# Optimization experiments

Hardware: AMD Instinct MI355X
Metric: run time of the kernel (lower is better)

The kernel has to match this reference:

```python
import jax, jax.numpy as jnp
import numpy as np

B, S, D_MODEL, NUM_HEADS, DFF = 4, 2048, 256, 8, 1024
DEPTH = D_MODEL // NUM_HEADS
EPS = 1e-6
LENGTH_SCALE = 1.0


def setup_inputs() -> dict:
    key = jax.random.key(0)
    ks = jax.random.split(key, 18)
    n = lambda k, shp, s=0.05: (jax.random.normal(k, shp, dtype=jnp.float32) * s)
    return {
        "x": jax.random.normal(ks[0], (B, S, D_MODEL), dtype=jnp.float32),
        "wq_w": n(ks[1], (D_MODEL, D_MODEL)), "wq_b": jnp.zeros((D_MODEL,), jnp.float32),
        "wk_w": n(ks[2], (D_MODEL, D_MODEL)), "wk_b": jnp.zeros((D_MODEL,), jnp.float32),
        "wv_w": n(ks[3], (D_MODEL, D_MODEL)), "wv_b": jnp.zeros((D_MODEL,), jnp.float32),
        "wo_w": n(ks[4], (D_MODEL, D_MODEL)), "wo_b": jnp.zeros((D_MODEL,), jnp.float32),
        "ffn1_w": n(ks[5], (D_MODEL, DFF)), "ffn1_b": jnp.zeros((DFF,), jnp.float32),
        "ffn2_w": n(ks[6], (DFF, D_MODEL)), "ffn2_b": jnp.zeros((D_MODEL,), jnp.float32),
        "ln1_g": jnp.ones((D_MODEL,), jnp.float32), "ln1_b": jnp.zeros((D_MODEL,), jnp.float32),
        "ln2_g": jnp.ones((D_MODEL,), jnp.float32), "ln2_b": jnp.zeros((D_MODEL,), jnp.float32),
    }


def _layernorm(x, g, b):
    mu = jnp.mean(x, axis=-1, keepdims=True)
    var = jnp.mean(jnp.square(x - mu), axis=-1, keepdims=True)
    return (x - mu) * jax.lax.rsqrt(var + EPS) * g + b


def _split_heads(t):
    # [B,S,D_MODEL] -> [B,H,S,depth]
    return t.reshape(B, S, NUM_HEADS, DEPTH).transpose(0, 2, 1, 3)


def _encoder_layer(x, wq_w, wq_b, wk_w, wk_b, wv_w, wv_b, wo_w, wo_b,
                   ffn1_w, ffn1_b, ffn2_w, ffn2_b, ln1_g, ln1_b, ln2_g, ln2_b):
    q = _split_heads(x @ wq_w + wq_b)
    k = _split_heads(x @ wk_w + wk_b)
    v = _split_heads(x @ wv_w + wv_b)
    # pairwise squared distances: ||q||^2 - 2 q.k + ||k||^2 -> [B,H,S,S]
    q2 = jnp.sum(q * q, axis=-1)  # [B,H,S]
    k2 = jnp.sum(k * k, axis=-1)  # [B,H,S]
    dists = q2[..., :, None] - 2.0 * jnp.einsum("bhqd,bhkd->bhqk", q, k) + k2[..., None, :]
    # exponentiated-quadratic kernel, then softmax over keys (mask=None)
    attn = jax.nn.softmax(jnp.exp(-0.5 * dists / (LENGTH_SCALE ** 2)), axis=-1)
    out = jnp.einsum("bhqk,bhkd->bhqd", attn, v)  # [B,H,S,depth]
    out = out.transpose(0, 2, 1, 3).reshape(B, S, D_MODEL)
    attn_out = out @ wo_w + wo_b
    # dropout is identity (training=False)
    out1 = _layernorm(x + attn_out, ln1_g, ln1_b)
    ffn = jax.nn.relu(out1 @ ffn1_w + ffn1_b) @ ffn2_w + ffn2_b
    return _layernorm(out1 + ffn, ln2_g, ln2_b)


def reference(x, wq_w, wq_b, wk_w, wk_b, wv_w, wv_b, wo_w, wo_b,
              ffn1_w, ffn1_b, ffn2_w, ffn2_b, ln1_g, ln1_b, ln2_g, ln2_b):
    return _encoder_layer(x, wq_w, wq_b, wk_w, wk_b, wv_w, wv_b, wo_w, wo_b,
                          ffn1_w, ffn1_b, ffn2_w, ffn2_b, ln1_g, ln1_b, ln2_g, ln2_b)
```

## Files before the change

kernel.cpp:

```cpp
#include <hip/hip_runtime.h>
#include <hip/hip_bf16.h>

#define SQL  2048
#define DM   256
#define LNEPS 1e-6f
#define LOG2E    (1.44269504f)

#define B_XB    (0ull)
#define B_QB    (4ull<<20)
#define B_KB    (8ull<<20)
#define B_VT    (12ull<<20)
#define B_CTX   (16ull<<20)
#define B_O1B   (20ull<<20)
#define B_O1F   (24ull<<20)
#define B_MID   (32ull<<20)
#define B_WQKVT (48ull<<20)
#define B_WOT   ((48ull<<20)+(512ull<<10))
#define B_W1T   (49ull<<20)
#define B_W2T   ((49ull<<20)+(512ull<<10))
#define B_BQKV  (50ull<<20)
#define B_HQ    ((50ull<<20)+(64ull<<10))
#define B_HK    ((50ull<<20)+(320ull<<10))
#define B_C2    (0ull)

typedef float  f32x16 __attribute__((ext_vector_type(16)));
typedef short  bf16x8 __attribute__((ext_vector_type(8)));
typedef int    i32x4  __attribute__((ext_vector_type(4)));
typedef int    i32x2  __attribute__((ext_vector_type(2)));

static __device__ __forceinline__ unsigned short bfu(float f){
    __hip_bfloat16 h = __float2bfloat16(f);
    return *reinterpret_cast<unsigned short*>(&h);
}
static __device__ __forceinline__ unsigned pk2(float a, float b){
    return (unsigned)bfu(a) | ((unsigned)bfu(b) << 16);
}
static __device__ __forceinline__ void glds16(const void* g, void* l){
    __builtin_amdgcn_global_load_lds((const __attribute__((address_space(1))) unsigned int*)g,
                                     (__attribute__((address_space(3))) unsigned int*)l, 16, 0, 0);
}

__global__ __launch_bounds__(256) void k_packall(
    const float* __restrict__ wq, const float* __restrict__ wk, const float* __restrict__ wv,
    const float* __restrict__ wo, const float* __restrict__ w1, const float* __restrict__ w2,
    const float* __restrict__ bq, const float* __restrict__ bk, const float* __restrict__ bv,
    const float* __restrict__ x,
    unsigned short* __restrict__ wqkvT, unsigned short* __restrict__ woT,
    unsigned short* __restrict__ w1T, unsigned short* __restrict__ w2T,
    float* __restrict__ bqkv, unsigned short* __restrict__ xb)
{
    __shared__ float tile[32][33];
    const int bid = blockIdx.x;
    const int t = threadIdx.x;
    if (bid < 768) {
        const float* W; unsigned short* Wt; int K, N, xk, yn;
        if (bid < 192) {
            int which = bid >> 6, local = bid & 63;
            W = (which == 0) ? wq : (which == 1 ? wk : wv);
            Wt = wqkvT + which * 65536; K = 256; N = 256;
            xk = local & 7; yn = local >> 3;
        } else if (bid < 256) {
            int local = bid - 192; W = wo; Wt = woT; K = 256; N = 256;
            xk = local & 7; yn = local >> 3;
        } else if (bid < 512) {
            int local = bid - 256; W = w1; Wt = w1T; K = 256; N = 1024;
            xk = local & 7; yn = local >> 3;
        } else {
            int local = bid - 512; W = w2; Wt = w2T; K = 1024; N = 256;
            xk = local & 31; yn = local >> 5;
        }
        const int tx = t & 31, ty = t >> 5;
        const int kb = xk * 32, nb = yn * 32;
#pragma unroll
        for (int i = 0; i < 32; i += 8) tile[ty + i][tx] = W[(size_t)(kb + ty + i) * N + nb + tx];
        __syncthreads();
#pragma unroll
        for (int i = 0; i < 32; i += 8) Wt[(size_t)(nb + ty + i) * K + kb + tx] = bfu(tile[tx][ty + i]);
    } else if (bid < 771) {
        int wb = bid - 768;
        const float* s = (wb == 0) ? bq : (wb == 1 ? bk : bv);
        bqkv[wb * 256 + t] = s[t];
    } else {
        const int i = (bid - 771) * 256 + t;
        float4 v = ((const float4*)x)[i];
        ushort4 o; o.x = bfu(v.x); o.y = bfu(v.y); o.z = bfu(v.z); o.w = bfu(v.w);
        ((ushort4*)xb)[i] = o;
    }
}

__global__ __launch_bounds__(256, 4) void k_qkv(
    const unsigned short* __restrict__ A, const unsigned short* __restrict__ Bt,
    const float* __restrict__ bias,
    unsigned short* __restrict__ qb, unsigned short* __restrict__ kb,
    char* __restrict__ vtg,
    unsigned int* __restrict__ hqp, unsigned int* __restrict__ hkp)
{
    __shared__ __align__(16) char As[8192];
    __shared__ __align__(16) char Bs[16384];
    const int t = threadIdx.x;
    const int lane = t & 63, w = t >> 6;
    const int lo = lane & 31, hi = lane >> 5;
    const int row0 = blockIdx.x * 64;
    const int col0 = blockIdx.y * 128;
    const int mr = (w & 1) * 32, nc = (w >> 1) * 64;
    f32x16 acc[2] = {};

    for (int kt = 0; kt < 4; ++kt) {
        const int k0 = kt * 64;
#pragma unroll
        for (int it = 0; it < 2; ++it) {
            const int idx = it * 256 + t;
            const int r = idx >> 3, g = idx & 7;
            glds16((const char*)(A + (size_t)(row0 + r) * 256 + k0) + ((g ^ (r & 7)) << 4),
                   As + it * 4096 + w * 1024 + lane * 16);
        }
#pragma unroll
        for (int it = 0; it < 4; ++it) {
            const int idx = it * 256 + t;
            const int r = idx >> 3, g = idx & 7;
            glds16((const char*)(Bt + (size_t)(col0 + r) * 256 + k0) + ((g ^ (r & 7)) << 4),
                   Bs + it * 4096 + w * 1024 + lane * 16);
        }
        __syncthreads();
        const int rA = mr + lo;
        const int rB = nc + lo;
#pragma unroll
        for (int s = 0; s < 4; ++s) {
            const int g = s * 2 + hi;
            bf16x8 fa  = *(const bf16x8*)(As + rA * 128 + ((g ^ (rA & 7)) << 4));
            bf16x8 fb0 = *(const bf16x8*)(Bs + rB * 128 + ((g ^ (rB & 7)) << 4));
            bf16x8 fb1 = *(const bf16x8*)(Bs + (rB + 32) * 128 + ((g ^ (rB & 7)) << 4));
            acc[0] = __builtin_amdgcn_mfma_f32_32x32x16_bf16(fa, fb0, acc[0], 0, 0, 0);
            acc[1] = __builtin_amdgcn_mfma_f32_32x32x16_bf16(fa, fb1, acc[1], 0, 0, 0);
        }
        __syncthreads();
    }
#pragma unroll
    for (int n = 0; n < 2; ++n) {
        const int c0 = col0 + nc + n * 32;
        const int which = c0 >> 8, h = (c0 >> 5) & 7;
        const float bv = bias[c0 + lo];
        if (which < 2) {
            unsigned short* dst = (which == 0) ? qb : kb;
            const float scl = (which == 0) ? LOG2E : 1.0f;
#pragma unroll
            for (int r = 0; r < 16; ++r) {
                const int gr = row0 + mr + (r & 3) + 8 * (r >> 2) + 4 * hi;
                const int b = gr >> 11, s = gr & 2047;
                const unsigned short u = bfu((acc[n][r] + bv) * scl);
                dst[(((size_t)(b * 8 + h)) * SQL + s) * 32 + lo] = u;
                const float vr = __builtin_bit_cast(float, ((unsigned)u) << 16);
                float sv = vr * vr;
                sv += __shfl_xor(sv, 1);  sv += __shfl_xor(sv, 2);
                sv += __shfl_xor(sv, 4);  sv += __shfl_xor(sv, 8);
                sv += __shfl_xor(sv, 16);
                if (lo == 0) {
                    const size_t gi = (size_t)(b * 8 + h) * SQL + s;
                    if (which == 0)
                        hqp[gi] = 0x3F80u | ((unsigned)bfu(-0.34657359f * sv + 0.52876637f) << 16);
                    else
                        hkp[gi] = (unsigned)bfu(-0.72134752f * sv) | 0x3F800000u;
                }
            }
        } else {
#pragma unroll
            for (int r = 0; r < 16; ++r) {
                const int gr = row0 + mr + (r & 3) + 8 * (r >> 2) + 4 * hi;
                const int b = gr >> 11, s = gr & 2047;
                const int o = s * 2;
                const int op = (o & ~0x78) | ((((o >> 3) & 15) ^ (lo & 15)) << 3);
                *(unsigned short*)(vtg + ((size_t)(b * 8 + h)) * 131072 + (size_t)lo * 4096 + op)
                    = bfu(acc[n][r] + bv);
            }
        }
    }
}

__global__ __launch_bounds__(512, 4) void k_attn(
    const unsigned short* __restrict__ qg, const unsigned short* __restrict__ kg,
    const char* __restrict__ vtg, const unsigned int* __restrict__ hqp,
    const unsigned int* __restrict__ hkp, unsigned short* __restrict__ ctxb)
{
    __shared__ __align__(16) char smem[34048];
    char* kls = smem;
    char* vtl = smem + 16384;
    float* hks  = (float*)(smem + 32768);
    float* invs = (float*)(smem + 33792);
    float* redacc = (float*)smem;
    float* redden = (float*)(smem + 24576);

    const int t = threadIdx.x;
    const int grp = t >> 7;
    const int tl  = t & 127;
    const int lane = t & 63;
    const int w   = (t >> 6) & 1;
    const int lo = lane & 31;
    const int hi = lane >> 5;

    const int bid = (blockIdx.x & 7) * 128 + (blockIdx.x >> 3);
    const int qc = bid & 31;
    const int bh = bid >> 5;

    const int qrow = qc * 64 + w * 32 + lo;
    const unsigned short* qp = qg + ((size_t)bh * SQL + qrow) * 32;
    const bf16x8 qf0 = *(const bf16x8*)(qp + hi * 8);
    const bf16x8 qf1 = *(const bf16x8*)(qp + 16 + hi * 8);
    i32x4 b3i = {};
    if (hi == 0) b3i[0] = (int)hqp[(size_t)bh * SQL + qrow];
    const bf16x8 b3 = __builtin_bit_cast(bf16x8, b3i);

    f32x16 acc = {};
    float den = 0.f;

    const unsigned short* kbg = kg + (size_t)bh * SQL * 32;
    const char* vtb = vtg + (size_t)bh * 131072;
    const unsigned int* hkb = hkp + (size_t)bh * SQL;
    char* kd = kls + grp * 4096;
    char* vd = vtl + grp * 4096;

    for (int kt = 0; kt < 8; ++kt) {
        const int key0 = grp * 512 + kt * 64;
        {
#pragma unroll
            for (int it = 0; it < 2; ++it) {
                const int idx = it * 128 + tl;
                const int r = idx >> 2, gl = idx & 3;
                glds16((const char*)(kbg + (size_t)(key0 + r) * 32) + ((gl ^ ((r >> 1) & 3)) << 4),
                       kd + idx * 16);
                const int vrw = idx >> 3, vch = idx & 7;
                glds16(vtb + (size_t)vrw * 4096 + key0 * 2 + vch * 16, vd + idx * 16);
            }
            if (tl < 64) hks[grp * 64 + tl] = __builtin_bit_cast(float, hkb[key0 + tl]);
        }
        __syncthreads();

#pragma unroll
        for (int h2 = 0; h2 < 2; ++h2) {
            const int kb32 = h2 * 32;
            const int kA = kb32 + lo;
            const char* krow = kd + kA * 64;
            const int ksw = (kA >> 1) & 3;
            bf16x8 kf0 = *(const bf16x8*)(krow + (((0 + hi) ^ ksw) << 4));
            bf16x8 kf1 = *(const bf16x8*)(krow + (((2 + hi) ^ ksw) << 4));
            i32x4 a3i = {};
            if (hi == 0) a3i[0] = __builtin_bit_cast(int, hks[grp * 64 + kA]);
            f32x16 sc = {};
            __builtin_amdgcn_s_setprio(1);
            sc = __builtin_amdgcn_mfma_f32_32x32x16_bf16(kf0, qf0, sc, 0, 0, 0);
            sc = __builtin_amdgcn_mfma_f32_32x32x16_bf16(kf1, qf1, sc, 0, 0, 0);
            sc = __builtin_amdgcn_mfma_f32_32x32x16_bf16(
                     __builtin_bit_cast(bf16x8, a3i), b3, sc, 0, 0, 0);
            __builtin_amdgcn_s_setprio(0);
            float wv[16];
#pragma unroll
            for (int r = 0; r < 16; ++r) {
                float e1 = __builtin_amdgcn_exp2f(sc[r]);
                float ww = __builtin_amdgcn_exp2f(e1);
                den += ww;
                wv[r] = ww;
            }
            i32x4 p0; p0[0]=pk2(wv[0],wv[1]);   p0[1]=pk2(wv[2],wv[3]);
                      p0[2]=pk2(wv[4],wv[5]);   p0[3]=pk2(wv[6],wv[7]);
            i32x4 p1; p1[0]=pk2(wv[8],wv[9]);   p1[1]=pk2(wv[10],wv[11]);
                      p1[2]=pk2(wv[12],wv[13]); p1[3]=pk2(wv[14],wv[15]);
            const char* vrow = vd + lo * 128;
            const int vxor = (lo & 15) << 3;
            const int o0 = (kb32 + 4 * hi) * 2;
            const int o1 = (kb32 + 16 + 4 * hi) * 2;
            i32x2 a0 = *(const i32x2*)(vrow + (o0 ^ vxor));
            i32x2 a1 = *(const i32x2*)(vrow + ((o0 + 16) ^ vxor));
            i32x2 b0 = *(const i32x2*)(vrow + (o1 ^ vxor));
            i32x2 b1 = *(const i32x2*)(vrow + ((o1 + 16) ^ vxor));
            i32x4 vb0; vb0[0]=a0[0]; vb0[1]=a0[1]; vb0[2]=a1[0]; vb0[3]=a1[1];
            i32x4 vb1; vb1[0]=b0[0]; vb1[1]=b0[1]; vb1[2]=b1[0]; vb1[3]=b1[1];
            __builtin_amdgcn_s_setprio(1);
            acc = __builtin_amdgcn_mfma_f32_32x32x16_bf16(
                __builtin_bit_cast(bf16x8, p0), __builtin_bit_cast(bf16x8, vb0), acc, 0, 0, 0);
            acc = __builtin_amdgcn_mfma_f32_32x32x16_bf16(
                __builtin_bit_cast(bf16x8, p1), __builtin_bit_cast(bf16x8, vb1), acc, 0, 0, 0);
            __builtin_amdgcn_s_setprio(0);
        }
        __syncthreads();
    }

    if (grp != 0) {
#pragma unroll
        for (int r = 0; r < 16; ++r) redacc[((grp - 1) * 16 + r) * 128 + tl] = acc[r];
        redden[(grp - 1) * 128 + tl] = den;
    }
    __syncthreads();
    if (grp == 0) {
#pragma unroll
        for (int r = 0; r < 16; ++r)
            acc[r] += redacc[r * 128 + tl] + redacc[(16 + r) * 128 + tl] + redacc[(32 + r) * 128 + tl];
        den += redden[tl] + redden[128 + tl] + redden[256 + tl];
        const float dfull = den + __shfl_xor(den, 32);
        if (hi == 0) invs[w * 32 + lo] = 1.f / dfull;
        float4 i0 = *(const float4*)&invs[w * 32 + 4 * hi];
        float4 i1 = *(const float4*)&invs[w * 32 + 8 + 4 * hi];
        float4 i2 = *(const float4*)&invs[w * 32 + 16 + 4 * hi];
        float4 i3 = *(const float4*)&invs[w * 32 + 24 + 4 * hi];
        float iv[16] = {i0.x,i0.y,i0.z,i0.w, i1.x,i1.y,i1.z,i1.w,
                        i2.x,i2.y,i2.z,i2.w, i3.x,i3.y,i3.z,i3.w};
        const int b = bh >> 3, h = bh & 7;
        unsigned short* cbase = ctxb + ((size_t)(b * SQL + qc * 64 + w * 32)) * 256 + h * 32 + lo;
#pragma unroll
        for (int r = 0; r < 16; ++r) {
            const int qr = (r & 3) + 8 * (r >> 2) + 4 * hi;
            cbase[(size_t)qr * 256] = bfu(acc[r] * iv[r]);
        }
    }
}

template<int KSTRIDE, int KT, int NFULL, int RELU, int OUTF, int OUTB>
__global__ __launch_bounds__(256, 6) void k_gemm(
    const unsigned short* __restrict__ A, const unsigned short* __restrict__ Bt,
    const float* __restrict__ bias,
    float* __restrict__ outf, unsigned short* __restrict__ outb)
{
    __shared__ __align__(16) char As[8192];
    __shared__ __align__(16) char Bs[16384];
    const int t = threadIdx.x;
    const int lane = t & 63, w = t >> 6;
    const int lo = lane & 31, hi = lane >> 5;
    const int row0 = blockIdx.x * 64;
    const int col0 = blockIdx.y * 128;
    const int mr = (w & 1) * 32, nc = (w >> 1) * 64;
    f32x16 acc[2] = {};

    for (int kt = 0; kt < KT; ++kt) {
        const int k0 = kt * 64;
#pragma unroll
        for (int it = 0; it < 2; ++it) {
            const int idx = it * 256 + t;
            const int r = idx >> 3, g = idx & 7;
            glds16((const char*)(A + (size_t)(row0 + r) * KSTRIDE + k0) + ((g ^ (r & 7)) << 4),
                   As + it * 4096 + w * 1024 + lane * 16);
        }
#pragma unroll
        for (int it = 0; it < 4; ++it) {
            const int idx = it * 256 + t;
            const int r = idx >> 3, g = idx & 7;
            glds16((const char*)(Bt + (size_t)(col0 + r) * KSTRIDE + k0) + ((g ^ (r & 7)) << 4),
                   Bs + it * 4096 + w * 1024 + lane * 16);
        }
        __syncthreads();
        const int rA = mr + lo;
        const int rB = nc + lo;
#pragma unroll
        for (int s = 0; s < 4; ++s) {
            const int g = s * 2 + hi;
            bf16x8 fa  = *(const bf16x8*)(As + rA * 128 + ((g ^ (rA & 7)) << 4));
            bf16x8 fb0 = *(const bf16x8*)(Bs + rB * 128 + ((g ^ (rB & 7)) << 4));
            bf16x8 fb1 = *(const bf16x8*)(Bs + (rB + 32) * 128 + ((g ^ (rB & 7)) << 4));
            acc[0] = __builtin_amdgcn_mfma_f32_32x32x16_bf16(fa, fb0, acc[0], 0, 0, 0);
            acc[1] = __builtin_amdgcn_mfma_f32_32x32x16_bf16(fa, fb1, acc[1], 0, 0, 0);
        }
        __syncthreads();
    }
#pragma unroll
    for (int n = 0; n < 2; ++n) {
        const int c0 = col0 + nc + n * 32;
        const float bv = bias[c0 + lo];
#pragma unroll
        for (int r = 0; r < 16; ++r) {
            const int gr = row0 + mr + (r & 3) + 8 * (r >> 2) + 4 * hi;
            float vv = acc[n][r] + bv;
            if (RELU) vv = fmaxf(vv, 0.f);
            if (OUTF) outf[(size_t)gr * NFULL + c0 + lo] = vv;
            if (OUTB) outb[(size_t)gr * NFULL + c0 + lo] = bfu(vv);
        }
    }
}

template<int DUAL>
__global__ __launch_bounds__(256) void k_lnsum(
    const float* __restrict__ pa, const float* __restrict__ res,
    const float* __restrict__ g, const float* __restrict__ bt,
    float* __restrict__ outf, unsigned short* __restrict__ outb)
{
    const int row = blockIdx.x * 4 + (threadIdx.x >> 6);
    const int lane = threadIdx.x & 63;
    const size_t base = (size_t)row * 256;
    float4 v  = ((const float4*)(pa + base))[lane];
    float4 v3 = ((const float4*)(res + base))[lane];
    v.x += v3.x; v.y += v3.y; v.z += v3.z; v.w += v3.w;
    float s  = v.x + v.y + v.z + v.w;
    float ss = v.x * v.x + v.y * v.y + v.z * v.z + v.w * v.w;
#pragma unroll
    for (int off = 32; off; off >>= 1) { s += __shfl_xor(s, off); ss += __shfl_xor(ss, off); }
    const float mu = s * (1.f / 256.f);
    const float rstd = rsqrtf(ss * (1.f / 256.f) - mu * mu + LNEPS);
    const float4 gg = ((const float4*)g)[lane];
    const float4 bb = ((const float4*)bt)[lane];
    float4 o;
    o.x = (v.x - mu) * rstd * gg.x + bb.x;
    o.y = (v.y - mu) * rstd * gg.y + bb.y;
    o.z = (v.z - mu) * rstd * gg.z + bb.z;
    o.w = (v.w - mu) * rstd * gg.w + bb.w;
    ((float4*)(outf + base))[lane] = o;
    if (DUAL) {
        ushort4 ob; ob.x = bfu(o.x); ob.y = bfu(o.y); ob.z = bfu(o.z); ob.w = bfu(o.w);
        ((ushort4*)(outb + base))[lane] = ob;
    }
}

extern "C" void kernel_launch(void* const* d_in, const int* in_sizes, int n_in,
                              void* d_out, int out_size, void* d_ws, size_t ws_size,
                              hipStream_t stream) {
    const float* x   = (const float*)d_in[0];
    const float* wq  = (const float*)d_in[1];  const float* bq  = (const float*)d_in[2];
    const float* wk  = (const float*)d_in[3];  const float* bk  = (const float*)d_in[4];
    const float* wv  = (const float*)d_in[5];  const float* bv  = (const float*)d_in[6];
    const float* wo  = (const float*)d_in[7];  const float* wob = (const float*)d_in[8];
    const float* w1  = (const float*)d_in[9];  const float* b1  = (const float*)d_in[10];
    const float* w2  = (const float*)d_in[11]; const float* b2  = (const float*)d_in[12];
    const float* g1  = (const float*)d_in[13]; const float* bl1 = (const float*)d_in[14];
    const float* g2  = (const float*)d_in[15]; const float* bl2 = (const float*)d_in[16];

    char* ws = (char*)d_ws;
    unsigned short* xb    = (unsigned short*)(ws + B_XB);
    unsigned short* qb    = (unsigned short*)(ws + B_QB);
    unsigned short* kbuf  = (unsigned short*)(ws + B_KB);
    char*           vt    = (char*)(ws + B_VT);
    unsigned short* ctxb  = (unsigned short*)(ws + B_CTX);
    unsigned short* o1b   = (unsigned short*)(ws + B_O1B);
    float*          o1f   = (float*)(ws + B_O1F);
    unsigned short* mid   = (unsigned short*)(ws + B_MID);
    float*          c1    = (float*)(ws + B_MID);
    float*          c2    = (float*)(ws + B_C2);
    unsigned short* wqkvT = (unsigned short*)(ws + B_WQKVT);
    unsigned short* woT   = (unsigned short*)(ws + B_WOT);
    unsigned short* w1T   = (unsigned short*)(ws + B_W1T);
    unsigned short* w2T   = (unsigned short*)(ws + B_W2T);
    float* bqkv = (float*)(ws + B_BQKV);
    unsigned int* hqp = (unsigned int*)(ws + B_HQ);
    unsigned int* hkp = (unsigned int*)(ws + B_HK);
    float* out  = (float*)d_out;

    k_packall<<<dim3(2819), dim3(256), 0, stream>>>(wq, wk, wv, wo, w1, w2, bq, bk, bv, x,
                                                    wqkvT, woT, w1T, w2T, bqkv, xb);
    k_qkv<<<dim3(128, 6), dim3(256), 0, stream>>>(xb, wqkvT, bqkv, qb, kbuf, vt, hqp, hkp);
    k_attn<<<dim3(1024), dim3(512), 0, stream>>>(qb, kbuf, vt, hqp, hkp, ctxb);
    k_gemm<256, 4, 256, 0, 1, 0><<<dim3(128, 2), dim3(256), 0, stream>>>(ctxb, woT, wob, c1, nullptr);
    k_lnsum<1><<<dim3(2048), dim3(256), 0, stream>>>(c1, x, g1, bl1, o1f, o1b);
    k_gemm<256, 4, 1024, 1, 0, 1><<<dim3(128, 8), dim3(256), 0, stream>>>(o1b, w1T, b1, nullptr, mid);
    k_gemm<1024, 16, 256, 0, 1, 0><<<dim3(128, 2), dim3(256), 0, stream>>>(mid, w2T, b2, c2, nullptr);
    k_lnsum<0><<<dim3(2048), dim3(256), 0, stream>>>(c2, o1f, g2, bl2, out, nullptr);
}
```

Before: 191.1 us.

## Fuse residual-add and LayerNorm into output-projection and FFN2 GEMM epilogues

Replaces the separate fp32 GEMM output plus row-LayerNorm kernels with a GEMM kernel whose blocks cover full 256-wide rows and compute bias, residual add and LayerNorm in the epilogue. This removes two launches and the fp32 intermediate write/read traffic. The second residual is now read from the bf16 copy of out1, reducing precision. The fused GEMMs launch only 128 blocks, lowering parallelism across the GPU.

```diff
diff --git a/kernel.cpp b/kernel.cpp
--- a/kernel.cpp
+++ b/kernel.cpp
@@ -12,7 +12,6 @@
 #define B_VT    (12ull<<20)
 #define B_CTX   (16ull<<20)
 #define B_O1B   (20ull<<20)
-#define B_O1F   (24ull<<20)
 #define B_MID   (32ull<<20)
 #define B_WQKVT (48ull<<20)
 #define B_WOT   ((48ull<<20)+(512ull<<10))
@@ -21,7 +20,6 @@
 #define B_BQKV  (50ull<<20)
 #define B_HQ    ((50ull<<20)+(64ull<<10))
 #define B_HK    ((50ull<<20)+(320ull<<10))
-#define B_C2    (0ull)
 
 typedef float  f32x16 __attribute__((ext_vector_type(16)));
 typedef short  bf16x8 __attribute__((ext_vector_type(8)));
@@ -31,6 +29,9 @@
 static __device__ __forceinline__ unsigned short bfu(float f){
     __hip_bfloat16 h = __float2bfloat16(f);
     return *reinterpret_cast<unsigned short*>(&h);
+}
+static __device__ __forceinline__ float b2f(unsigned short u){
+    return __builtin_bit_cast(float, ((unsigned)u) << 16);
 }
 static __device__ __forceinline__ unsigned pk2(float a, float b){
     return (unsigned)bfu(a) | ((unsigned)bfu(b) << 16);
@@ -112,14 +113,14 @@
             const int idx = it * 256 + t;
             const int r = idx >> 3, g = idx & 7;
             glds16((const char*)(A + (size_t)(row0 + r) * 256 + k0) + ((g ^ (r & 7)) << 4),
-                   As + it * 4096 + w * 1024 + lane * 16);
+                   As + idx * 16);
         }
 #pragma unroll
         for (int it = 0; it < 4; ++it) {
             const int idx = it * 256 + t;
             const int r = idx >> 3, g = idx & 7;
             glds16((const char*)(Bt + (size_t)(col0 + r) * 256 + k0) + ((g ^ (r & 7)) << 4),
-                   Bs + it * 4096 + w * 1024 + lane * 16);
+                   Bs + idx * 16);
         }
         __syncthreads();
         const int rA = mr + lo;
@@ -149,7 +150,7 @@
                 const int b = gr >> 11, s = gr & 2047;
                 const unsigned short u = bfu((acc[n][r] + bv) * scl);
                 dst[(((size_t)(b * 8 + h)) * SQL + s) * 32 + lo] = u;
-                const float vr = __builtin_bit_cast(float, ((unsigned)u) << 16);
+                const float vr = b2f(u);
                 float sv = vr * vr;
                 sv += __shfl_xor(sv, 1);  sv += __shfl_xor(sv, 2);
                 sv += __shfl_xor(sv, 4);  sv += __shfl_xor(sv, 8);
@@ -312,11 +313,117 @@
     }
 }
 
-template<int KSTRIDE, int KT, int NFULL, int RELU, int OUTF, int OUTB>
+template<int KDIM, int RES_BF, int OUT_BF>
+__global__ __launch_bounds__(256, 2) void k_gemm_ln(
+    const unsigned short* __restrict__ A, const unsigned short* __restrict__ Bt,
+    const float* __restrict__ bias, const void* __restrict__ resid,
+    const float* __restrict__ g, const float* __restrict__ bt,
+    float* __restrict__ outf, unsigned short* __restrict__ outb)
+{
+    __shared__ __align__(16) char As[8192];
+    __shared__ __align__(16) char Bs[32768];
+    __shared__ float lnred[64][4];
+    const int t = threadIdx.x;
+    const int lane = t & 63, w = t >> 6;
+    const int lo = lane & 31, hi = lane >> 5;
+    const int wm = w & 1, wn = w >> 1;
+    const int row0 = blockIdx.x * 64;
+    f32x16 acc[4] = {};
+
+    for (int kt = 0; kt < KDIM / 64; ++kt) {
+        const int k0 = kt * 64;
+#pragma unroll
+        for (int it = 0; it < 2; ++it) {
+            const int idx = it * 256 + t;
+            const int r = idx >> 3, gg = idx & 7;
+            glds16((const char*)(A + (size_t)(row0 + r) * KDIM + k0) + ((gg ^ (r & 7)) << 4),
+                   As + idx * 16);
+        }
+#pragma unroll
+        for (int it = 0; it < 8; ++it) {
+            const int idx = it * 256 + t;
+            const int r = idx >> 3, gg = idx & 7;
+            glds16((const char*)(Bt + (size_t)r * KDIM + k0) + ((gg ^ (r & 7)) << 4),
+                   Bs + idx * 16);
+        }
+        __syncthreads();
+        const int rA = wm * 32 + lo;
+#pragma unroll
+        for (int s = 0; s < 4; ++s) {
+            const int gg = s * 2 + hi;
+            bf16x8 fa = *(const bf16x8*)(As + rA * 128 + ((gg ^ (rA & 7)) << 4));
+#pragma unroll
+            for (int n = 0; n < 4; ++n) {
+                const int rB = wn * 128 + n * 32 + lo;
+                bf16x8 fb = *(const bf16x8*)(Bs + rB * 128 + ((gg ^ (rB & 7)) << 4));
+                acc[n] = __builtin_amdgcn_mfma_f32_32x32x16_bf16(fa, fb, acc[n], 0, 0, 0);
+            }
+        }
+        __syncthreads();
+    }
+
+    float vals[4][16];
+    float s_[16], ss_[16];
+#pragma unroll
+    for (int r = 0; r < 16; ++r) { s_[r] = 0.f; ss_[r] = 0.f; }
+#pragma unroll
+    for (int n = 0; n < 4; ++n) {
+        const int c = wn * 128 + n * 32 + lo;
+        const float bv = bias[c];
+#pragma unroll
+        for (int r = 0; r < 16; ++r) {
+            const int gr = row0 + wm * 32 + (r & 3) + 8 * (r >> 2) + 4 * hi;
+            float rv;
+            if (RES_BF) rv = b2f(((const unsigned short*)resid)[(size_t)gr * 256 + c]);
+            else        rv = ((const float*)resid)[(size_t)gr * 256 + c];
+            float v = acc[n][r] + bv + rv;
+            vals[n][r] = v;
+            s_[r] += v; ss_[r] += v * v;
+        }
+    }
+#pragma unroll
+    for (int r = 0; r < 16; ++r) {
+#pragma unroll
+        for (int off = 16; off; off >>= 1) {
+            s_[r]  += __shfl_xor(s_[r],  off);
+            ss_[r] += __shfl_xor(ss_[r], off);
+        }
+    }
+    if (lo == 0) {
+#pragma unroll
+        for (int r = 0; r < 16; ++r) {
+            const int row = wm * 32 + (r & 3) + 8 * (r >> 2) + 4 * hi;
+            lnred[row][wn * 2]     = s_[r];
+            lnred[row][wn * 2 + 1] = ss_[r];
+        }
+    }
+    __syncthreads();
+    float mu_[16], rs_[16];
+#pragma unroll
+    for (int r = 0; r < 16; ++r) {
+        const int row = wm * 32 + (r & 3) + 8 * (r >> 2) + 4 * hi;
+        const float mu = (lnred[row][0] + lnred[row][2]) * (1.f / 256.f);
+        const float va = (lnred[row][1] + lnred[row][3]) * (1.f / 256.f) - mu * mu;
+        mu_[r] = mu; rs_[r] = rsqrtf(va + LNEPS);
+    }
+#pragma unroll
+    for (int n = 0; n < 4; ++n) {
+        const int c = wn * 128 + n * 32 + lo;
+        const float gv = g[c], bv = bt[c];
+#pragma unroll
+        for (int r = 0; r < 16; ++r) {
+            const int gr = row0 + wm * 32 + (r & 3) + 8 * (r >> 2) + 4 * hi;
+            const float o = (vals[n][r] - mu_[r]) * rs_[r] * gv + bv;
+            if (OUT_BF) outb[(size_t)gr * 256 + c] = bfu(o);
+            else        outf[(size_t)gr * 256 + c] = o;
+        }
+    }
+}
+
+template<int KSTRIDE, int KT, int NFULL, int RELU>
 __global__ __launch_bounds__(256, 6) void k_gemm(
     const unsigned short* __restrict__ A, const unsigned short* __restrict__ Bt,
-    const float* __restrict__ bias,
-    float* __restrict__ outf, unsigned short* __restrict__ outb)
+    const float* __restrict__ bias, unsigned short* __restrict__ outb)
 {
     __shared__ __align__(16) char As[8192];
     __shared__ __align__(16) char Bs[16384];
@@ -335,14 +442,14 @@
             const int idx = it * 256 + t;
             const int r = idx >> 3, g = idx & 7;
             glds16((const char*)(A + (size_t)(row0 + r) * KSTRIDE + k0) + ((g ^ (r & 7)) << 4),
-                   As + it * 4096 + w * 1024 + lane * 16);
+                   As + idx * 16);
         }
 #pragma unroll
         for (int it = 0; it < 4; ++it) {
             const int idx = it * 256 + t;
             const int r = idx >> 3, g = idx & 7;
             glds16((const char*)(Bt + (size_t)(col0 + r) * KSTRIDE + k0) + ((g ^ (r & 7)) << 4),
-                   Bs + it * 4096 + w * 1024 + lane * 16);
+                   Bs + idx * 16);
         }
         __syncthreads();
         const int rA = mr + lo;
@@ -367,41 +474,8 @@
             const int gr = row0 + mr + (r & 3) + 8 * (r >> 2) + 4 * hi;
             float vv = acc[n][r] + bv;
             if (RELU) vv = fmaxf(vv, 0.f);
-            if (OUTF) outf[(size_t)gr * NFULL + c0 + lo] = vv;
-            if (OUTB) outb[(size_t)gr * NFULL + c0 + lo] = bfu(vv);
-        }
-    }
-}
-
-template<int DUAL>
-__global__ __launch_bounds__(256) void k_lnsum(
-    const float* __restrict__ pa, const float* __restrict__ res,
-    const float* __restrict__ g, const float* __restrict__ bt,
-    float* __restrict__ outf, unsigned short* __restrict__ outb)
-{
-    const int row = blockIdx.x * 4 + (threadIdx.x >> 6);
-    const int lane = threadIdx.x & 63;
-    const size_t base = (size_t)row * 256;
-    float4 v  = ((const float4*)(pa + base))[lane];
-    float4 v3 = ((const float4*)(res + base))[lane];
-    v.x += v3.x; v.y += v3.y; v.z += v3.z; v.w += v3.w;
-    float s  = v.x + v.y + v.z + v.w;
-    float ss = v.x * v.x + v.y * v.y + v.z * v.z + v.w * v.w;
-#pragma unroll
-    for (int off = 32; off; off >>= 1) { s += __shfl_xor(s, off); ss += __shfl_xor(ss, off); }
-    const float mu = s * (1.f / 256.f);
-    const float rstd = rsqrtf(ss * (1.f / 256.f) - mu * mu + LNEPS);
-    const float4 gg = ((const float4*)g)[lane];
-    const float4 bb = ((const float4*)bt)[lane];
-    float4 o;
-    o.x = (v.x - mu) * rstd * gg.x + bb.x;
-    o.y = (v.y - mu) * rstd * gg.y + bb.y;
-    o.z = (v.z - mu) * rstd * gg.z + bb.z;
-    o.w = (v.w - mu) * rstd * gg.w + bb.w;
-    ((float4*)(outf + base))[lane] = o;
-    if (DUAL) {
-        ushort4 ob; ob.x = bfu(o.x); ob.y = bfu(o.y); ob.z = bfu(o.z); ob.w = bfu(o.w);
-        ((ushort4*)(outb + base))[lane] = ob;
+            outb[(size_t)gr * NFULL + c0 + lo] = bfu(vv);
+        }
     }
 }
 
@@ -425,10 +499,7 @@
     char*           vt    = (char*)(ws + B_VT);
     unsigned short* ctxb  = (unsigned short*)(ws + B_CTX);
     unsigned short* o1b   = (unsigned short*)(ws + B_O1B);
-    float*          o1f   = (float*)(ws + B_O1F);
     unsigned short* mid   = (unsigned short*)(ws + B_MID);
-    float*          c1    = (float*)(ws + B_MID);
-    float*          c2    = (float*)(ws + B_C2);
     unsigned short* wqkvT = (unsigned short*)(ws + B_WQKVT);
     unsigned short* woT   = (unsigned short*)(ws + B_WOT);
     unsigned short* w1T   = (unsigned short*)(ws + B_W1T);
@@ -442,9 +513,9 @@
                                                     wqkvT, woT, w1T, w2T, bqkv, xb);
     k_qkv<<<dim3(128, 6), dim3(256), 0, stream>>>(xb, wqkvT, bqkv, qb, kbuf, vt, hqp, hkp);
     k_attn<<<dim3(1024), dim3(512), 0, stream>>>(qb, kbuf, vt, hqp, hkp, ctxb);
-    k_gemm<256, 4, 256, 0, 1, 0><<<dim3(128, 2), dim3(256), 0, stream>>>(ctxb, woT, wob, c1, nullptr);
-    k_lnsum<1><<<dim3(2048), dim3(256), 0, stream>>>(c1, x, g1, bl1, o1f, o1b);
-    k_gemm<256, 4, 1024, 1, 0, 1><<<dim3(128, 8), dim3(256), 0, stream>>>(o1b, w1T, b1, nullptr, mid);
-    k_gemm<1024, 16, 256, 0, 1, 0><<<dim3(128, 2), dim3(256), 0, stream>>>(mid, w2T, b2, c2, nullptr);
-    k_lnsum<0><<<dim3(2048), dim3(256), 0, stream>>>(c2, o1f, g2, bl2, out, nullptr);
-}
+    k_gemm_ln<256, 0, 1><<<dim3(128), dim3(256), 0, stream>>>(
+        ctxb, woT, wob, x, g1, bl1, nullptr, o1b);
+    k_gemm<256, 4, 1024, 1><<<dim3(128, 8), dim3(256), 0, stream>>>(o1b, w1T, b1, mid);
+    k_gemm_ln<1024, 1, 0><<<dim3(128), dim3(256), 0, stream>>>(
+        mid, w2T, b2, o1b, g2, bl2, out, nullptr);
+}
```

Measured after the change: 199.1 us. 1.04x slower.
